# Performance work log

Measured on AMD Instinct MI355X. Metric: run time of the kernel, lower is better.

## Reference

```python
import jax, jax.numpy as jnp
import numpy as np

DIM = 512
CODEBOOK_SIZE = 16384
CODEBOOK_DIM = 14  # log2(CODEBOOK_SIZE)
CODEBOOK_SCALE = 1.0
INV_TEMPERATURE = 100.0
ENTROPY_LOSS_WEIGHT = 0.1
COMMITMENT_LOSS_WEIGHT = 0.25
DIVERSITY_GAMMA = 1.0
EPS = 1e-5


def _bit_mask():
    # mask buffer: 2**[cd-1 .. 0]
    return (2 ** jnp.arange(CODEBOOK_DIM - 1, -1, -1)).astype(jnp.int32)


def _make_codebook():
    codes = jnp.arange(CODEBOOK_SIZE, dtype=jnp.int32)
    bits = ((codes[:, None] & _bit_mask()) != 0).astype(jnp.float32)  # [J, cd]
    return bits * (2.0 * CODEBOOK_SCALE) - CODEBOOK_SCALE


def setup_inputs() -> dict:
    key = jax.random.key(0)
    ks = jax.random.split(key, 5)
    b, n = 4, 2048
    bound_in = 1.0 / np.sqrt(DIM)
    bound_out = 1.0 / np.sqrt(CODEBOOK_DIM)
    x = jax.random.normal(ks[0], (b, n, DIM), dtype=jnp.float32)
    W_in = jax.random.uniform(ks[1], (CODEBOOK_DIM, DIM), jnp.float32, -bound_in, bound_in)
    b_in = jax.random.uniform(ks[2], (CODEBOOK_DIM,), jnp.float32, -bound_in, bound_in)
    W_out = jax.random.uniform(ks[3], (DIM, CODEBOOK_DIM), jnp.float32, -bound_out, bound_out)
    b_out = jax.random.uniform(ks[4], (DIM,), jnp.float32, -bound_out, bound_out)
    codebook = _make_codebook()  # buffer, deterministic
    return {"x": x, "W_in": W_in, "b_in": b_in, "W_out": W_out, "b_out": b_out, "codebook": codebook}


def _entropy(prob):
    return jnp.sum(-prob * jnp.log(jnp.clip(prob, EPS)), axis=-1)


def reference(x, W_in, b_in, W_out, b_out, codebook):
    # project_in: [b, n, dim] -> [b, n, cd] (num_codebooks == 1, so c-dim is implicit)
    h = jnp.einsum('bnd,cd->bnc', x, W_in) + b_in
    original_input = h

    # per-bit sign quantization
    quantized = jnp.where(h > 0, CODEBOOK_SCALE, -CODEBOOK_SCALE).astype(h.dtype)
    # straight-through estimator (training mode)
    h_st = h + jax.lax.stop_gradient(quantized - h)

    # indices: bits -> integer codes, [b, n]
    indices = jnp.sum((h_st > 0).astype(jnp.int32) * _bit_mask(), axis=-1)

    # entropy aux loss: softmax(-distance * inv_temp), distance = -2 <orig, code>
    logits = (2.0 * INV_TEMPERATURE) * jnp.einsum('bnd,jd->bnj', original_input, codebook)
    prob = jax.nn.softmax(logits, axis=-1)  # [b, n, J]
    per_sample_entropy = jnp.mean(_entropy(prob))
    avg_prob = jnp.mean(prob, axis=(0, 1))  # [J]
    codebook_entropy = _entropy(avg_prob)
    entropy_aux_loss = per_sample_entropy - DIVERSITY_GAMMA * codebook_entropy

    # commitment loss
    commit_loss = jnp.mean((original_input - jax.lax.stop_gradient(quantized)) ** 2)

    # project_out: [b, n, cd] -> [b, n, dim]
    out = jnp.einsum('bnc,dc->bnd', h_st, W_out) + b_out

    aux_loss = entropy_aux_loss * ENTROPY_LOSS_WEIGHT + commit_loss * COMMITMENT_LOSS_WEIGHT
    return out, indices, aux_loss
```

## Files before the change

### kernel.cpp

```cpp
#include <hip/hip_runtime.h>
#include <math.h>

#define DIM 512
#define CD 14
#define NCODES 16384
#define NTOK 8192
#define EPS 1e-5f
#define LOG_EPS -11.5129254650f
#define PTHRESH 1e-12f

#define WS_ENT 16384
#define WS_COM (16384 + 2048)
#define WS_H   (16384 + 4096)
#define NBLK_H 1792
#define NBLK_Z 64
#define NBLK_PS (NTOK / 4)
#define WT_S 513

__global__ __launch_bounds__(256) void k_h(
    const float* __restrict__ x, const float* __restrict__ W_in,
    const float* __restrict__ b_in, float* __restrict__ ws)
{
#pragma clang fp contract(off)
    const int tid = threadIdx.x;
    if (blockIdx.x >= NBLK_H) {
        ws[(blockIdx.x - NBLK_H) * 256 + tid] = 0.f;
        return;
    }
    const int gid = blockIdx.x * 256 + tid;
    const int dot = gid >> 2;
    const int j   = gid & 3;
    const int t = dot / CD;
    const int c = dot - t * CD;
    const float* xp = x + (size_t)t * DIM + j;
    const float* wp = W_in + (size_t)c * DIM + j;

    float a = 0.f;
    #pragma unroll 4
    for (int i = 0; i < 32; ++i) {
        const int base = i * 16;
        const float x3 = xp[base + 12], w3 = wp[base + 12];
        const float x2 = xp[base + 8],  w2 = wp[base + 8];
        const float x1 = xp[base + 4],  w1 = wp[base + 4];
        const float x0 = xp[base + 0],  w0 = wp[base + 0];
        a = (x3 * w3) + a;
        a = (x2 * w2) + a;
        a = (x1 * w1) + a;
        a = (x0 * w0) + a;
    }
    const float s2  = a + __shfl_xor(a, 1);
    const float sum = s2 + __shfl_xor(s2, 2);
    if (j == 0) ws[WS_H + (size_t)t * 16 + c] = sum + b_in[c];
}

__global__ __launch_bounds__(256) void k_ps(
    const float* __restrict__ hbuf, const float* __restrict__ W_out,
    const float* __restrict__ b_out, float* __restrict__ out,
    float* __restrict__ idx_out, float* __restrict__ ws)
{
    __shared__ float wT[CD * WT_S];
    __shared__ float h_lds[4][16];
    __shared__ float f_lds[4][16];
    __shared__ float entred[4], comred[4];

    const int tid  = threadIdx.x;
    const int wave = tid >> 6, lane = tid & 63;
    const int tok  = blockIdx.x * 4 + wave;

    #pragma unroll
    for (int i = 0; i < 7; ++i) {
        const int e = (i * 256 + tid) * 4;
        const float4 v = *(const float4*)(W_out + e);
        {const int idx = e + 0; const int d = idx / CD; wT[(idx - d * CD) * WT_S + d] = v.x;}
        {const int idx = e + 1; const int d = idx / CD; wT[(idx - d * CD) * WT_S + d] = v.y;}
        {const int idx = e + 2; const int d = idx / CD; wT[(idx - d * CD) * WT_S + d] = v.z;}
        {const int idx = e + 3; const int d = idx / CD; wT[(idx - d * CD) * WT_S + d] = v.w;}
    }
    if (lane < CD) {
        const float hv = hbuf[(size_t)tok * 16 + lane];
        h_lds[wave][lane] = hv;
        f_lds[wave][lane] = __expf(-400.f * fabsf(hv));
    }
    __syncthreads();

    float s[CD];
    int jstar = 0;
    #pragma unroll
    for (int c = 0; c < CD; ++c) {
        const bool pos = h_lds[wave][c] > 0.f;
        s[c] = pos ? 1.f : -1.f;
        jstar |= (pos ? 1 : 0) << (13 - c);
    }
    if (lane == 0) idx_out[tok] = (float)jstar;

    #pragma unroll
    for (int r = 0; r < 8; ++r) {
        const int d = r * 64 + lane;
        float v = b_out[d];
        #pragma unroll
        for (int c = 0; c < CD; ++c) v = fmaf(s[c], wT[c * WT_S + d], v);
        out[(size_t)tok * DIM + d] = v;
    }

    float Z = 1.f, commit = 0.f;
    int hot = 0;
    #pragma unroll
    for (int c = 0; c < CD; ++c) {
        const float fv = f_lds[wave][c];
        const float ah = fabsf(h_lds[wave][c]);
        const float dd = ah - 1.f;
        commit = fmaf(dd, dd, commit);
        Z *= 1.f + fv;
        hot |= (fv >= PTHRESH ? 1 : 0) << c;
    }
    const float invZ = 1.f / Z;
    const int nmask = 1 << __popc(hot);

    float ent = 0.f;
    for (int base = 0; base < nmask; base += 64) {
        const int si = base + lane;
        float prod = 1.f;
        int flip = 0, pos = 0;
        #pragma unroll
        for (int c = 0; c < CD; ++c) {
            if ((hot >> c) & 1) {
                if ((si >> pos) & 1) {
                    prod *= f_lds[wave][c];
                    flip |= 1 << (13 - c);
                }
                ++pos;
            }
        }
        if (si < nmask) {
            const float p = prod * invZ;
            if (p >= PTHRESH) {
                ent = fmaf(p, fmaxf(__logf(p), LOG_EPS) - LOG_EPS, ent);
                atomicAdd(&ws[jstar ^ flip], p);
            }
        }
    }
    #pragma unroll
    for (int off = 32; off; off >>= 1) ent += __shfl_xor(ent, off);
    if (lane == 0) { entred[wave] = ent; comred[wave] = commit; }
    __syncthreads();
    if (tid == 0) {
        ws[WS_ENT + blockIdx.x] = (entred[0] + entred[1]) + (entred[2] + entred[3]);
        ws[WS_COM + blockIdx.x] = (comred[0] + comred[1]) + (comred[2] + comred[3]);
    }
}

__global__ __launch_bounds__(1024) void k_final(
    const float* __restrict__ ws, float* __restrict__ aux_out)
{
    __shared__ float r1[1024], r2[1024], r3[1024];
    const int tid = threadIdx.x;
    float acc = 0.f;
    #pragma unroll
    for (int k = 0; k < 16; ++k) {
        const float ap = ws[tid + k * 1024] * (1.f / 8192.f);
        acc = fmaf(ap, __logf(fmaxf(ap, EPS)), acc);
    }
    float entp = ws[WS_ENT + tid] + ws[WS_ENT + tid + 1024];
    float comp = ws[WS_COM + tid] + ws[WS_COM + tid + 1024];
    r1[tid] = acc; r2[tid] = entp; r3[tid] = comp;
    __syncthreads();
    for (int s = 512; s > 0; s >>= 1) {
        if (tid < s) {
            r1[tid] += r1[tid + s];
            r2[tid] += r2[tid + s];
            r3[tid] += r3[tid + s];
        }
        __syncthreads();
    }
    if (tid == 0) {
        const float cbH = -r1[0];
        const float psH = -(r2[0] * (1.f / 8192.f) + LOG_EPS);
        const float commit = r3[0] * (1.f / (8192.f * 14.f));
        aux_out[0] = (psH - cbH) * 0.1f + commit * 0.25f;
    }
}

extern "C" void kernel_launch(void* const* d_in, const int* in_sizes, int n_in,
                              void* d_out, int out_size, void* d_ws, size_t ws_size,
                              hipStream_t stream) {
    const float* x     = (const float*)d_in[0];
    const float* W_in  = (const float*)d_in[1];
    const float* b_in  = (const float*)d_in[2];
    const float* W_out = (const float*)d_in[3];
    const float* b_out = (const float*)d_in[4];

    float* out     = (float*)d_out;
    float* idx_out = out + (size_t)NTOK * DIM;
    float* aux_out = idx_out + NTOK;
    float* ws      = (float*)d_ws;

    hipLaunchKernelGGL(k_h, dim3(NBLK_H + NBLK_Z), dim3(256), 0, stream,
                       x, W_in, b_in, ws);
    hipLaunchKernelGGL(k_ps, dim3(NBLK_PS), dim3(256), 0, stream,
                       ws + WS_H, W_out, b_out, out, idx_out, ws);
    hipLaunchKernelGGL(k_final, dim3(1), dim3(1024), 0, stream, ws, aux_out);
}
```

Before: 54.16 us.

## Fuse input projection into main kernel and read W_out directly from global

Merges the h-projection kernel into the per-token kernel, so each block computes its 4 tokens' 14-dim projections into shared memory instead of round-tripping them through the workspace. It drops the per-block LDS transpose of W_out and reads W_out rows as float2 straight from global/cache, and zeroes the histogram with hipMemsetAsync. This removes one launch, the global h buffer and 28KB of LDS per block. In exchange only 224 of 256 threads do the projection, and the W_out reads are strided per lane (56-byte stride), which may coalesce worse.

```diff
diff --git a/kernel.cpp b/kernel.cpp
--- a/kernel.cpp
+++ b/kernel.cpp
@@ -11,77 +11,55 @@
 
 #define WS_ENT 16384
 #define WS_COM (16384 + 2048)
-#define WS_H   (16384 + 4096)
-#define NBLK_H 1792
-#define NBLK_Z 64
-#define NBLK_PS (NTOK / 4)
-#define WT_S 513
+#define NBLK (NTOK / 4)
 
-__global__ __launch_bounds__(256) void k_h(
+__global__ __launch_bounds__(256) void k_main(
     const float* __restrict__ x, const float* __restrict__ W_in,
-    const float* __restrict__ b_in, float* __restrict__ ws)
-{
-#pragma clang fp contract(off)
-    const int tid = threadIdx.x;
-    if (blockIdx.x >= NBLK_H) {
-        ws[(blockIdx.x - NBLK_H) * 256 + tid] = 0.f;
-        return;
-    }
-    const int gid = blockIdx.x * 256 + tid;
-    const int dot = gid >> 2;
-    const int j   = gid & 3;
-    const int t = dot / CD;
-    const int c = dot - t * CD;
-    const float* xp = x + (size_t)t * DIM + j;
-    const float* wp = W_in + (size_t)c * DIM + j;
-
-    float a = 0.f;
-    #pragma unroll 4
-    for (int i = 0; i < 32; ++i) {
-        const int base = i * 16;
-        const float x3 = xp[base + 12], w3 = wp[base + 12];
-        const float x2 = xp[base + 8],  w2 = wp[base + 8];
-        const float x1 = xp[base + 4],  w1 = wp[base + 4];
-        const float x0 = xp[base + 0],  w0 = wp[base + 0];
-        a = (x3 * w3) + a;
-        a = (x2 * w2) + a;
-        a = (x1 * w1) + a;
-        a = (x0 * w0) + a;
-    }
-    const float s2  = a + __shfl_xor(a, 1);
-    const float sum = s2 + __shfl_xor(s2, 2);
-    if (j == 0) ws[WS_H + (size_t)t * 16 + c] = sum + b_in[c];
-}
-
-__global__ __launch_bounds__(256) void k_ps(
-    const float* __restrict__ hbuf, const float* __restrict__ W_out,
+    const float* __restrict__ b_in, const float* __restrict__ W_out,
     const float* __restrict__ b_out, float* __restrict__ out,
     float* __restrict__ idx_out, float* __restrict__ ws)
 {
-    __shared__ float wT[CD * WT_S];
+#pragma clang fp contract(off)
     __shared__ float h_lds[4][16];
     __shared__ float f_lds[4][16];
     __shared__ float entred[4], comred[4];
 
     const int tid  = threadIdx.x;
     const int wave = tid >> 6, lane = tid & 63;
-    const int tok  = blockIdx.x * 4 + wave;
 
-    #pragma unroll
-    for (int i = 0; i < 7; ++i) {
-        const int e = (i * 256 + tid) * 4;
-        const float4 v = *(const float4*)(W_out + e);
-        {const int idx = e + 0; const int d = idx / CD; wT[(idx - d * CD) * WT_S + d] = v.x;}
-        {const int idx = e + 1; const int d = idx / CD; wT[(idx - d * CD) * WT_S + d] = v.y;}
-        {const int idx = e + 2; const int d = idx / CD; wT[(idx - d * CD) * WT_S + d] = v.z;}
-        {const int idx = e + 3; const int d = idx / CD; wT[(idx - d * CD) * WT_S + d] = v.w;}
-    }
-    if (lane < CD) {
-        const float hv = hbuf[(size_t)tok * 16 + lane];
-        h_lds[wave][lane] = hv;
-        f_lds[wave][lane] = __expf(-400.f * fabsf(hv));
+    const int dot = tid >> 2;
+    const int j   = tid & 3;
+    if (dot < 4 * CD) {
+        const int tt = dot / CD;
+        const int c  = dot - tt * CD;
+        const int t  = blockIdx.x * 4 + tt;
+        const float* xp = x + (size_t)t * DIM + j;
+        const float* wp = W_in + (size_t)c * DIM + j;
+
+        float a = 0.f;
+        #pragma unroll 4
+        for (int i = 0; i < 32; ++i) {
+            const int base = i * 16;
+            const float x3 = xp[base + 12], w3 = wp[base + 12];
+            const float x2 = xp[base + 8],  w2 = wp[base + 8];
+            const float x1 = xp[base + 4],  w1 = wp[base + 4];
+            const float x0 = xp[base + 0],  w0 = wp[base + 0];
+            a = (x3 * w3) + a;
+            a = (x2 * w2) + a;
+            a = (x1 * w1) + a;
+            a = (x0 * w0) + a;
+        }
+        const float s2  = a + __shfl_xor(a, 1);
+        const float sum = s2 + __shfl_xor(s2, 2);
+        if (j == 0) {
+            const float hv = sum + b_in[c];
+            h_lds[tt][c] = hv;
+            f_lds[tt][c] = __expf(-400.f * fabsf(hv));
+        }
     }
     __syncthreads();
+
+    const int tok = blockIdx.x * 4 + wave;
 
     float s[CD];
     int jstar = 0;
@@ -96,9 +74,14 @@
     #pragma unroll
     for (int r = 0; r < 8; ++r) {
         const int d = r * 64 + lane;
+        const float2* wp2 = (const float2*)(W_out + (size_t)d * CD);
         float v = b_out[d];
         #pragma unroll
-        for (int c = 0; c < CD; ++c) v = fmaf(s[c], wT[c * WT_S + d], v);
+        for (int q = 0; q < 7; ++q) {
+            const float2 w = wp2[q];
+            v = fmaf(s[2 * q],     w.x, v);
+            v = fmaf(s[2 * q + 1], w.y, v);
+        }
         out[(size_t)tok * DIM + d] = v;
     }
 
@@ -194,9 +177,8 @@
     float* aux_out = idx_out + NTOK;
     float* ws      = (float*)d_ws;
 
-    hipLaunchKernelGGL(k_h, dim3(NBLK_H + NBLK_Z), dim3(256), 0, stream,
-                       x, W_in, b_in, ws);
-    hipLaunchKernelGGL(k_ps, dim3(NBLK_PS), dim3(256), 0, stream,
-                       ws + WS_H, W_out, b_out, out, idx_out, ws);
+    hipMemsetAsync(ws, 0, NCODES * sizeof(float), stream);
+    hipLaunchKernelGGL(k_main, dim3(NBLK), dim3(256), 0, stream,
+                       x, W_in, b_in, W_out, b_out, out, idx_out, ws);
     hipLaunchKernelGGL(k_final, dim3(1), dim3(1024), 0, stream, ws, aux_out);
 }
```

New measurement: 60.17 us. +11.1%, slower.
